# Optimization experiments

Hardware: AMD Instinct MI355X
Metric: run time of the kernel (lower is better)

Reference implementation:

```python
import jax, jax.numpy as jnp
import numpy as np

B, C, H, W = 8, 128, 64, 64


def setup_inputs() -> dict:
    key = jax.random.key(0)
    ks = jax.random.split(key, 4)
    s = 1.0 / np.sqrt(C)
    return {
        "x": jax.random.normal(ks[0], (B, C, H, W), dtype=jnp.float32),
        "Wq": jax.random.normal(ks[1], (C, C), dtype=jnp.float32) * s,
        "bq": jnp.zeros((C,), dtype=jnp.float32),
        "Wk": jax.random.normal(ks[2], (C, C), dtype=jnp.float32) * s,
        "bk": jnp.zeros((C,), dtype=jnp.float32),
        "Wv": jax.random.normal(ks[3], (C, C), dtype=jnp.float32) * s,
        "bv": jnp.zeros((C,), dtype=jnp.float32),
    }


def reference(x, Wq, bq, Wk, bk, Wv, bv):
    b, c, h, w = x.shape
    xf = x.reshape(b, c, h * w)  # [B, C, N]
    # 1x1 convs are per-pixel CxC matmuls (weight[out,in] contracted over in)
    q = jnp.einsum("oc,bcn->bon", Wq, xf) + bq[None, :, None]
    k = jnp.einsum("oc,bcn->bon", Wk, xf) + bk[None, :, None]
    v = jnp.einsum("oc,bcn->bon", Wv, xf) + bv[None, :, None]
    scale = 1.0 / jnp.sqrt(jnp.asarray(c, dtype=x.dtype))
    attn = jnp.einsum("bcn,bcm->bnm", q, k) * scale  # [B, N, N]
    attn = jax.nn.softmax(attn, axis=-1)
    out = jnp.einsum("bnm,bcm->bcn", attn, v)  # [B, C, N]
    return out.reshape(b, c, h, w) + x
```

## Files before the change

### kernel.cpp

```cpp
#include <hip/hip_runtime.h>

#define B_ 8
#define C_ 128
#define N_ 4096
#define SCALE 0.08838834764831845f

typedef __attribute__((ext_vector_type(8))) short short8;
typedef __attribute__((ext_vector_type(4))) short short4v;
typedef __attribute__((ext_vector_type(4))) float f32x4;

__device__ inline unsigned short f2b(float f) {
    unsigned int u;
    asm("v_cvt_pk_bf16_f32 %0, %1, %2" : "=v"(u) : "v"(f), "v"(f));
    return (unsigned short)u;
}

__device__ inline void gld_lds16(const void* g, void* l) {
    __builtin_amdgcn_global_load_lds(
        (const __attribute__((address_space(1))) unsigned int*)g,
        (__attribute__((address_space(3))) unsigned int*)l, 16, 0, 0);
}

__global__ __launch_bounds__(512) void kv_mfma(
    const float* __restrict__ x,
    const float* __restrict__ Wk, const float* __restrict__ bk,
    const float* __restrict__ Wv, const float* __restrict__ bv,
    unsigned short* __restrict__ kTs, unsigned short* __restrict__ vS)
{
    __shared__ __align__(16) short Xs[64 * 128];
    __shared__ __align__(16) float Obuf[64 * 132];

    const int t    = threadIdx.x;
    const int w    = t >> 6;
    const int lane = t & 63;
    const int l15  = lane & 15;
    const int quad = lane >> 4;

    const int b  = blockIdx.x & 7;
    const int n0 = (blockIdx.x >> 3) * 64;
    const long base = (long)b * C_ * N_;

    auto load_af = [&](const float* __restrict__ W, short8 (&af)[4]) {
        const int o = 16 * w + l15;
        #pragma unroll
        for (int ks = 0; ks < 4; ++ks) {
            const float4 a0 = *(const float4*)(const void*)(W + o * C_ + ks * 32 + quad * 8);
            const float4 a1 = *(const float4*)(const void*)(W + o * C_ + ks * 32 + quad * 8 + 4);
            union { unsigned int u[4]; short8 s; } pk;
            asm("v_cvt_pk_bf16_f32 %0, %1, %2" : "=v"(pk.u[0]) : "v"(a0.x), "v"(a0.y));
            asm("v_cvt_pk_bf16_f32 %0, %1, %2" : "=v"(pk.u[1]) : "v"(a0.z), "v"(a0.w));
            asm("v_cvt_pk_bf16_f32 %0, %1, %2" : "=v"(pk.u[2]) : "v"(a1.x), "v"(a1.y));
            asm("v_cvt_pk_bf16_f32 %0, %1, %2" : "=v"(pk.u[3]) : "v"(a1.z), "v"(a1.w));
            af[ks] = pk.s;
        }
    };

    auto mfma_pass = [&](const short8 (&af)[4], f32x4 (&acc)[4]) {
        #pragma unroll
        for (int nt = 0; nt < 4; ++nt) acc[nt] = (f32x4){0.f, 0.f, 0.f, 0.f};
        #pragma unroll
        for (int nt = 0; nt < 4; ++nt) {
            const int n = nt * 16 + l15;
            #pragma unroll
            for (int ks = 0; ks < 4; ++ks) {
                const short8 bx = *(const short8*)(const void*)(Xs + n * 128 + (((ks * 4 + quad) ^ l15) << 3));
                acc[nt] = __builtin_amdgcn_mfma_f32_16x16x32_bf16(af[ks], bx, acc[nt], 0, 0, 0);
            }
        }
    };

    short8 afA[4], afB[4];
    load_af(Wv, afA);

    #pragma unroll
    for (int it = 0; it < 4; ++it) {
        const int c  = (t >> 4) + it * 32;
        const int n4 = (t & 15) * 4;
        const float4 xv = *(const float4*)(const void*)(x + base + (long)c * N_ + n0 + n4);
        const int bc = c >> 3, cl = c & 7;
        Xs[(n4 + 0) * 128 + ((bc ^ ((n4 + 0) & 15)) << 3) + cl] = (short)f2b(xv.x);
        Xs[(n4 + 1) * 128 + ((bc ^ ((n4 + 1) & 15)) << 3) + cl] = (short)f2b(xv.y);
        Xs[(n4 + 2) * 128 + ((bc ^ ((n4 + 2) & 15)) << 3) + cl] = (short)f2b(xv.z);
        Xs[(n4 + 3) * 128 + ((bc ^ ((n4 + 3) & 15)) << 3) + cl] = (short)f2b(xv.w);
    }
    __syncthreads();

    {
        load_af(Wk, afB);
        f32x4 acc[4];
        mfma_pass(afA, acc);
        #pragma unroll
        for (int r = 0; r < 4; ++r) {
            const int o = 16 * w + quad * 4 + r;
            const float bb = bv[o];
            const int sw = ((o >> 1) & 3) << 3;
            #pragma unroll
            for (int nt = 0; nt < 4; ++nt) {
                const int n = nt * 16 + l15;
                const int ns = (n & 32) | ((((n >> 3) & 3) << 3) ^ sw) | (n & 7);
                vS[base + (long)o * N_ + n0 + ns] = f2b(acc[nt][r] + bb);
            }
        }
    }

    {
        f32x4 acc[4];
        mfma_pass(afB, acc);
        #pragma unroll
        for (int r = 0; r < 4; ++r) {
            const int o = 16 * w + quad * 4 + r;
            const float bb = bk[o];
            #pragma unroll
            for (int nt = 0; nt < 4; ++nt) {
                const int n = nt * 16 + l15;
                Obuf[n * 132 + (((o >> 3) ^ l15) << 3) + (o & 7)] = acc[nt][r] + bb;
            }
        }
        __syncthreads();
        const int n = t >> 3, oh = (t & 7) * 16;
        #pragma unroll
        for (int i = 0; i < 16; i += 8) {
            const float4 k0 = *(const float4*)(const void*)(Obuf + n * 132 + oh + i);
            const float4 k1 = *(const float4*)(const void*)(Obuf + n * 132 + oh + i + 4);
            union { unsigned int u[4]; short8 s; } pk;
            asm("v_cvt_pk_bf16_f32 %0, %1, %2" : "=v"(pk.u[0]) : "v"(k0.x), "v"(k0.y));
            asm("v_cvt_pk_bf16_f32 %0, %1, %2" : "=v"(pk.u[1]) : "v"(k0.z), "v"(k0.w));
            asm("v_cvt_pk_bf16_f32 %0, %1, %2" : "=v"(pk.u[2]) : "v"(k1.x), "v"(k1.y));
            asm("v_cvt_pk_bf16_f32 %0, %1, %2" : "=v"(pk.u[3]) : "v"(k1.z), "v"(k1.w));
            *(short8*)(void*)(kTs + base + (long)(n0 + n) * C_ + oh + i) = pk.s;
        }
    }
}

__global__ __launch_bounds__(512, 4) void attn_mfma(
    const float* __restrict__ Wq, const float* __restrict__ bq,
    const unsigned short* __restrict__ kTs,
    const unsigned short* __restrict__ vS,
    const float* __restrict__ xg,
    float* out)
{
    __shared__ union {
        struct {
            short V[2][2][4096];
            short Pb[2][2][2][32 * 40];
        } s;
        struct {
            short Xst[64 * 128];
            short Qs[64 * 128];
        } pre;
        float Ot[64 * 130];
    } sm;
    __shared__ float Ls[2][2][32];
    __shared__ float linvA[64];

    const int t    = threadIdx.x;
    const int w    = t >> 6;
    const int g    = w >> 2;
    const int wq   = (w >> 1) & 1;
    const int h    = w & 1;
    const int sub  = w & 3;
    const int lane = t & 63;
    const int l15  = lane & 15;
    const int quad = lane >> 4;

    const int b  = blockIdx.x & 7;
    const int n0 = (blockIdx.x >> 3) * 64;
    const long base = (long)b * C_ * N_;

    #pragma unroll
    for (int it = 0; it < 4; ++it) {
        const int c  = (t >> 4) + it * 32;
        const int n4 = (t & 15) * 4;
        const float4 xv = *(const float4*)(const void*)(xg + base + (long)c * N_ + n0 + n4);
        const int bc = c >> 3, cl = c & 7;
        sm.pre.Xst[(n4 + 0) * 128 + ((bc ^ ((n4 + 0) & 15)) << 3) + cl] = (short)f2b(xv.x);
        sm.pre.Xst[(n4 + 1) * 128 + ((bc ^ ((n4 + 1) & 15)) << 3) + cl] = (short)f2b(xv.y);
        sm.pre.Xst[(n4 + 2) * 128 + ((bc ^ ((n4 + 2) & 15)) << 3) + cl] = (short)f2b(xv.z);
        sm.pre.Xst[(n4 + 3) * 128 + ((bc ^ ((n4 + 3) & 15)) << 3) + cl] = (short)f2b(xv.w);
    }
    __syncthreads();
    {
        short8 aq[4];
        const int o = 16 * w + l15;
        #pragma unroll
        for (int ks = 0; ks < 4; ++ks) {
            const float4 a0 = *(const float4*)(const void*)(Wq + o * C_ + ks * 32 + quad * 8);
            const float4 a1 = *(const float4*)(const void*)(Wq + o * C_ + ks * 32 + quad * 8 + 4);
            union { unsigned int u[4]; short8 s; } pk;
            asm("v_cvt_pk_bf16_f32 %0, %1, %2" : "=v"(pk.u[0]) : "v"(a0.x), "v"(a0.y));
            asm("v_cvt_pk_bf16_f32 %0, %1, %2" : "=v"(pk.u[1]) : "v"(a0.z), "v"(a0.w));
            asm("v_cvt_pk_bf16_f32 %0, %1, %2" : "=v"(pk.u[2]) : "v"(a1.x), "v"(a1.y));
            asm("v_cvt_pk_bf16_f32 %0, %1, %2" : "=v"(pk.u[3]) : "v"(a1.z), "v"(a1.w));
            aq[ks] = pk.s;
        }
        f32x4 qa[4];
        #pragma unroll
        for (int nt = 0; nt < 4; ++nt) qa[nt] = (f32x4){0.f, 0.f, 0.f, 0.f};
        #pragma unroll
        for (int nt = 0; nt < 4; ++nt) {
            const int n = nt * 16 + l15;
            #pragma unroll
            for (int ks = 0; ks < 4; ++ks) {
                const short8 bx = *(const short8*)(const void*)(
                    sm.pre.Xst + n * 128 + (((ks * 4 + quad) ^ l15) << 3));
                qa[nt] = __builtin_amdgcn_mfma_f32_16x16x32_bf16(aq[ks], bx, qa[nt], 0, 0, 0);
            }
        }
        const float4 bb = *(const float4*)(const void*)(bq + 16 * w + quad * 4);
        #pragma unroll
        for (int r = 0; r < 4; ++r) {
            const int oo = 16 * w + quad * 4 + r;
            const float br = r == 0 ? bb.x : r == 1 ? bb.y : r == 2 ? bb.z : bb.w;
            #pragma unroll
            for (int nt = 0; nt < 4; ++nt) {
                const int n = nt * 16 + l15;
                sm.pre.Qs[n * 128 + (((oo >> 3) ^ (n & 15)) << 3) + (oo & 7)] =
                    (short)f2b((qa[nt][r] + br) * SCALE);
            }
        }
    }
    __syncthreads();

    short8 qf[2][4];
    #pragma unroll
    for (int qh = 0; qh < 2; ++qh)
        #pragma unroll
        for (int ks = 0; ks < 4; ++ks) {
            const int query = 32 * wq + qh * 16 + l15;
            qf[qh][ks] = *(const short8*)(const void*)(
                sm.pre.Qs + query * 128 + (((ks * 4 + quad) ^ l15) << 3));
        }

    f32x4 acc[2][4];
    #pragma unroll
    for (int qh = 0; qh < 2; ++qh)
        #pragma unroll
        for (int ct = 0; ct < 4; ++ct) acc[qh][ct] = (f32x4){0.f, 0.f, 0.f, 0.f};
    f32x4 accS[2];
    accS[0] = (f32x4){0.f, 0.f, 0.f, 0.f};
    accS[1] = (f32x4){0.f, 0.f, 0.f, 0.f};
    short8 ones;
    #pragma unroll
    for (int j = 0; j < 8; ++j) ones[j] = (short)0x3F80;

    auto stageV = [&](int buf, int pair) {
        const int mt = pair * 2 + g;
        char* lV = (char*)sm.s.V[buf][g];
        #pragma unroll
        for (int jj = 0; jj < 2; ++jj) {
            const int d  = sub * 2048 + jj * 1024;
            const int dv = d + lane * 16;
            const int c  = dv >> 6;
            gld_lds16((const char*)(vS + base + (long)c * N_ + mt * 32) + (dv & 63), lV + d);
        }
    };

    const unsigned short* kp = kTs + base + (long)((g * 32 + h * 16 + l15) * C_);
    int ko[4];
    #pragma unroll
    for (int ks = 0; ks < 4; ++ks) ko[ks] = (((ks * 4 + quad) ^ l15) << 3);
    short8 kf[4];

    stageV(0, 0);
    #pragma unroll
    for (int ks = 0; ks < 4; ++ks) kf[ks] = *(const short8*)(const void*)(kp + ko[ks]);
    kp += 64 * C_;

    for (int i = 0; i < 64; ++i) {
        f32x4 sc[2];
        sc[0] = (f32x4){0.f, 0.f, 0.f, 0.f};
        sc[1] = (f32x4){0.f, 0.f, 0.f, 0.f};
        __builtin_amdgcn_s_setprio(1);
        #pragma unroll
        for (int qh = 0; qh < 2; ++qh)
            #pragma unroll
            for (int ks = 0; ks < 4; ++ks)
                sc[qh] = __builtin_amdgcn_mfma_f32_16x16x32_bf16(qf[qh][ks], kf[ks], sc[qh], 0, 0, 0);
        __builtin_amdgcn_s_setprio(0);

        if (i < 63) {
            #pragma unroll
            for (int ks = 0; ks < 4; ++ks) kf[ks] = *(const short8*)(const void*)(kp + ko[ks]);
            kp += 64 * C_;
        }

        short* Pw = sm.s.Pb[i & 1][g][wq];
        #pragma unroll
        for (int qh = 0; qh < 2; ++qh)
            #pragma unroll
            for (int r = 0; r < 4; ++r)
                Pw[(qh * 16 + quad * 4 + r) * 40 + h * 16 + l15] = (short)f2b(__expf(sc[qh][r]));

        if (i < 63) asm volatile("s_waitcnt vmcnt(4)" ::: "memory");
        else        asm volatile("s_waitcnt vmcnt(0)" ::: "memory");
        asm volatile("s_waitcnt lgkmcnt(0)" ::: "memory");
        __builtin_amdgcn_s_barrier();
        __builtin_amdgcn_sched_barrier(0);

        if (i < 63) stageV((i + 1) & 1, i + 1);

        const short* Vb = sm.s.V[i & 1][g];
        const short8 pf0 = *(const short8*)(const void*)(Pw + (l15) * 40 + quad * 8);
        const short8 pf1 = *(const short8*)(const void*)(Pw + (16 + l15) * 40 + quad * 8);
        __builtin_amdgcn_s_setprio(1);
        if (h == 0) {
            accS[0] = __builtin_amdgcn_mfma_f32_16x16x32_bf16(pf0, ones, accS[0], 0, 0, 0);
            accS[1] = __builtin_amdgcn_mfma_f32_16x16x32_bf16(pf1, ones, accS[1], 0, 0, 0);
        }
        #pragma unroll
        for (int ct = 0; ct < 4; ++ct) {
            const int ch = h * 64 + ct * 16 + l15;
            const short8 vf = *(const short8*)(const void*)(Vb + ch * 32 + ((quad ^ ((l15 >> 1) & 3)) << 3));
            acc[0][ct] = __builtin_amdgcn_mfma_f32_16x16x32_bf16(pf0, vf, acc[0][ct], 0, 0, 0);
            acc[1][ct] = __builtin_amdgcn_mfma_f32_16x16x32_bf16(pf1, vf, acc[1][ct], 0, 0, 0);
        }
        __builtin_amdgcn_s_setprio(0);
    }

    if (h == 0 && l15 == 0) {
        #pragma unroll
        for (int qh = 0; qh < 2; ++qh)
            #pragma unroll
            for (int r = 0; r < 4; ++r)
                Ls[g][wq][qh * 16 + quad * 4 + r] = accS[qh][r];
    }
    __syncthreads();
    if (g == 0) {
        #pragma unroll
        for (int qh = 0; qh < 2; ++qh)
            #pragma unroll
            for (int ct = 0; ct < 4; ++ct)
                #pragma unroll
                for (int r = 0; r < 4; ++r)
                    sm.Ot[(32 * wq + qh * 16 + quad * 4 + r) * 130 + h * 64 + ct * 16 + l15] = acc[qh][ct][r];
    }
    __syncthreads();
    if (g == 1) {
        #pragma unroll
        for (int qh = 0; qh < 2; ++qh)
            #pragma unroll
            for (int ct = 0; ct < 4; ++ct)
                #pragma unroll
                for (int r = 0; r < 4; ++r)
                    sm.Ot[(32 * wq + qh * 16 + quad * 4 + r) * 130 + h * 64 + ct * 16 + l15] += acc[qh][ct][r];
    } else if (h == 0 && l15 == 0) {
        #pragma unroll
        for (int qh = 0; qh < 2; ++qh)
            #pragma unroll
            for (int r = 0; r < 4; ++r) {
                const int r32 = qh * 16 + quad * 4 + r;
                linvA[32 * wq + r32] = 1.0f / fmaxf(Ls[0][wq][r32] + Ls[1][wq][r32], 1e-20f);
            }
    }
    __syncthreads();

    const int c  = t >> 2;
    const int nh = (t & 3) * 16;
    const long gb = base + (long)c * N_ + n0 + nh;
    #pragma unroll
    for (int i = 0; i < 16; i += 4) {
        const float4 xs = *(const float4*)(const void*)(xg + gb + i);
        float4 rv;
        rv.x = sm.Ot[(nh + i + 0) * 130 + c] * linvA[nh + i + 0] + xs.x;
        rv.y = sm.Ot[(nh + i + 1) * 130 + c] * linvA[nh + i + 1] + xs.y;
        rv.z = sm.Ot[(nh + i + 2) * 130 + c] * linvA[nh + i + 2] + xs.z;
        rv.w = sm.Ot[(nh + i + 3) * 130 + c] * linvA[nh + i + 3] + xs.w;
        *(float4*)(void*)(out + gb + i) = rv;
    }
}

extern "C" void kernel_launch(void* const* d_in, const int* in_sizes, int n_in,
                              void* d_out, int out_size, void* d_ws, size_t ws_size,
                              hipStream_t stream) {
    const float* x  = (const float*)d_in[0];
    const float* Wq = (const float*)d_in[1];
    const float* bq = (const float*)d_in[2];
    const float* Wk = (const float*)d_in[3];
    const float* bk = (const float*)d_in[4];
    const float* Wv = (const float*)d_in[5];
    const float* bv = (const float*)d_in[6];
    float* out = (float*)d_out;

    const long BCN = (long)B_ * C_ * N_;
    unsigned short* kTs = (unsigned short*)d_ws;
    unsigned short* vS  = kTs + BCN;

    kv_mfma<<<512, 512, 0, stream>>>(x, Wk, bk, Wv, bv, kTs, vS);
    attn_mfma<<<B_ * (N_ / 64), 512, 0, stream>>>(Wq, bq, kTs, vS, x, out);
}
```

Measured before the change: 185.5 us.

## Fuse K/V projection and attention into one kernel with grid barrier

Merges the K/V projection kernel and the attention kernel into a single persistent launch of 512 blocks. Each block converts its x tile to bf16 once and reuses it for the K, V and Q projections, then all blocks meet at an atomic-counter grid barrier before attention begins. This saves a kernel launch and the second load and conversion of x, but adds a memset launch, a global spin barrier, and a dependency on all 512 blocks being resident at once to avoid deadlock.

```diff
diff --git a/kernel.cpp b/kernel.cpp
--- a/kernel.cpp
+++ b/kernel.cpp
@@ -4,6 +4,7 @@
 #define C_ 128
 #define N_ 4096
 #define SCALE 0.08838834764831845f
+#define NBLK 512u
 
 typedef __attribute__((ext_vector_type(8))) short short8;
 typedef __attribute__((ext_vector_type(4))) short short4v;
@@ -21,17 +22,38 @@
         (__attribute__((address_space(3))) unsigned int*)l, 16, 0, 0);
 }
 
-__global__ __launch_bounds__(512) void kv_mfma(
+__global__ __launch_bounds__(512, 4) void fused_attn(
     const float* __restrict__ x,
+    const float* __restrict__ Wq, const float* __restrict__ bq,
     const float* __restrict__ Wk, const float* __restrict__ bk,
     const float* __restrict__ Wv, const float* __restrict__ bv,
-    unsigned short* __restrict__ kTs, unsigned short* __restrict__ vS)
+    unsigned short* __restrict__ kTs, unsigned short* __restrict__ vS,
+    unsigned int* gsync,
+    float* __restrict__ out)
 {
-    __shared__ __align__(16) short Xs[64 * 128];
-    __shared__ __align__(16) float Obuf[64 * 132];
+    __shared__ __align__(16) union {
+        struct {
+            short Xs[64 * 128];
+            union {
+                float Obuf[64 * 132];
+                short Qs[64 * 128];
+            } o;
+        } p;
+        struct {
+            short V[2][2][4096];
+            short Pb[2][2][2][32 * 40];
+        } s;
+        float Ot[64 * 130];
+    } sm;
+    __shared__ float Ls[2][2][32];
+    __shared__ float linvA[64];
 
     const int t    = threadIdx.x;
     const int w    = t >> 6;
+    const int g    = w >> 2;
+    const int wq   = (w >> 1) & 1;
+    const int h    = w & 1;
+    const int sub  = w & 3;
     const int lane = t & 63;
     const int l15  = lane & 15;
     const int quad = lane >> 4;
@@ -63,7 +85,8 @@
             const int n = nt * 16 + l15;
             #pragma unroll
             for (int ks = 0; ks < 4; ++ks) {
-                const short8 bx = *(const short8*)(const void*)(Xs + n * 128 + (((ks * 4 + quad) ^ l15) << 3));
+                const short8 bx = *(const short8*)(const void*)(
+                    sm.p.Xs + n * 128 + (((ks * 4 + quad) ^ l15) << 3));
                 acc[nt] = __builtin_amdgcn_mfma_f32_16x16x32_bf16(af[ks], bx, acc[nt], 0, 0, 0);
             }
         }
@@ -78,10 +101,10 @@
         const int n4 = (t & 15) * 4;
         const float4 xv = *(const float4*)(const void*)(x + base + (long)c * N_ + n0 + n4);
         const int bc = c >> 3, cl = c & 7;
-        Xs[(n4 + 0) * 128 + ((bc ^ ((n4 + 0) & 15)) << 3) + cl] = (short)f2b(xv.x);
-        Xs[(n4 + 1) * 128 + ((bc ^ ((n4 + 1) & 15)) << 3) + cl] = (short)f2b(xv.y);
-        Xs[(n4 + 2) * 128 + ((bc ^ ((n4 + 2) & 15)) << 3) + cl] = (short)f2b(xv.z);
-        Xs[(n4 + 3) * 128 + ((bc ^ ((n4 + 3) & 15)) << 3) + cl] = (short)f2b(xv.w);
+        sm.p.Xs[(n4 + 0) * 128 + ((bc ^ ((n4 + 0) & 15)) << 3) + cl] = (short)f2b(xv.x);
+        sm.p.Xs[(n4 + 1) * 128 + ((bc ^ ((n4 + 1) & 15)) << 3) + cl] = (short)f2b(xv.y);
+        sm.p.Xs[(n4 + 2) * 128 + ((bc ^ ((n4 + 2) & 15)) << 3) + cl] = (short)f2b(xv.z);
+        sm.p.Xs[(n4 + 3) * 128 + ((bc ^ ((n4 + 3) & 15)) << 3) + cl] = (short)f2b(xv.w);
     }
     __syncthreads();
 
@@ -113,15 +136,15 @@
             #pragma unroll
             for (int nt = 0; nt < 4; ++nt) {
                 const int n = nt * 16 + l15;
-                Obuf[n * 132 + (((o >> 3) ^ l15) << 3) + (o & 7)] = acc[nt][r] + bb;
+                sm.p.o.Obuf[n * 132 + (((o >> 3) ^ l15) << 3) + (o & 7)] = acc[nt][r] + bb;
             }
         }
         __syncthreads();
         const int n = t >> 3, oh = (t & 7) * 16;
         #pragma unroll
         for (int i = 0; i < 16; i += 8) {
-            const float4 k0 = *(const float4*)(const void*)(Obuf + n * 132 + oh + i);
-            const float4 k1 = *(const float4*)(const void*)(Obuf + n * 132 + oh + i + 4);
+            const float4 k0 = *(const float4*)(const void*)(sm.p.o.Obuf + n * 132 + oh + i);
+            const float4 k1 = *(const float4*)(const void*)(sm.p.o.Obuf + n * 132 + oh + i + 4);
             union { unsigned int u[4]; short8 s; } pk;
             asm("v_cvt_pk_bf16_f32 %0, %1, %2" : "=v"(pk.u[0]) : "v"(k0.x), "v"(k0.y));
             asm("v_cvt_pk_bf16_f32 %0, %1, %2" : "=v"(pk.u[1]) : "v"(k0.z), "v"(k0.w));
@@ -130,69 +153,11 @@
             *(short8*)(void*)(kTs + base + (long)(n0 + n) * C_ + oh + i) = pk.s;
         }
     }
-}
-
-__global__ __launch_bounds__(512, 4) void attn_mfma(
-    const float* __restrict__ Wq, const float* __restrict__ bq,
-    const unsigned short* __restrict__ kTs,
-    const unsigned short* __restrict__ vS,
-    const float* __restrict__ xg,
-    float* out)
-{
-    __shared__ union {
-        struct {
-            short V[2][2][4096];
-            short Pb[2][2][2][32 * 40];
-        } s;
-        struct {
-            short Xst[64 * 128];
-            short Qs[64 * 128];
-        } pre;
-        float Ot[64 * 130];
-    } sm;
-    __shared__ float Ls[2][2][32];
-    __shared__ float linvA[64];
-
-    const int t    = threadIdx.x;
-    const int w    = t >> 6;
-    const int g    = w >> 2;
-    const int wq   = (w >> 1) & 1;
-    const int h    = w & 1;
-    const int sub  = w & 3;
-    const int lane = t & 63;
-    const int l15  = lane & 15;
-    const int quad = lane >> 4;
-
-    const int b  = blockIdx.x & 7;
-    const int n0 = (blockIdx.x >> 3) * 64;
-    const long base = (long)b * C_ * N_;
-
-    #pragma unroll
-    for (int it = 0; it < 4; ++it) {
-        const int c  = (t >> 4) + it * 32;
-        const int n4 = (t & 15) * 4;
-        const float4 xv = *(const float4*)(const void*)(xg + base + (long)c * N_ + n0 + n4);
-        const int bc = c >> 3, cl = c & 7;
-        sm.pre.Xst[(n4 + 0) * 128 + ((bc ^ ((n4 + 0) & 15)) << 3) + cl] = (short)f2b(xv.x);
-        sm.pre.Xst[(n4 + 1) * 128 + ((bc ^ ((n4 + 1) & 15)) << 3) + cl] = (short)f2b(xv.y);
-        sm.pre.Xst[(n4 + 2) * 128 + ((bc ^ ((n4 + 2) & 15)) << 3) + cl] = (short)f2b(xv.z);
-        sm.pre.Xst[(n4 + 3) * 128 + ((bc ^ ((n4 + 3) & 15)) << 3) + cl] = (short)f2b(xv.w);
-    }
-    __syncthreads();
+    __syncthreads();
+
     {
         short8 aq[4];
-        const int o = 16 * w + l15;
-        #pragma unroll
-        for (int ks = 0; ks < 4; ++ks) {
-            const float4 a0 = *(const float4*)(const void*)(Wq + o * C_ + ks * 32 + quad * 8);
-            const float4 a1 = *(const float4*)(const void*)(Wq + o * C_ + ks * 32 + quad * 8 + 4);
-            union { unsigned int u[4]; short8 s; } pk;
-            asm("v_cvt_pk_bf16_f32 %0, %1, %2" : "=v"(pk.u[0]) : "v"(a0.x), "v"(a0.y));
-            asm("v_cvt_pk_bf16_f32 %0, %1, %2" : "=v"(pk.u[1]) : "v"(a0.z), "v"(a0.w));
-            asm("v_cvt_pk_bf16_f32 %0, %1, %2" : "=v"(pk.u[2]) : "v"(a1.x), "v"(a1.y));
-            asm("v_cvt_pk_bf16_f32 %0, %1, %2" : "=v"(pk.u[3]) : "v"(a1.z), "v"(a1.w));
-            aq[ks] = pk.s;
-        }
+        load_af(Wq, aq);
         f32x4 qa[4];
         #pragma unroll
         for (int nt = 0; nt < 4; ++nt) qa[nt] = (f32x4){0.f, 0.f, 0.f, 0.f};
@@ -202,7 +167,7 @@
             #pragma unroll
             for (int ks = 0; ks < 4; ++ks) {
                 const short8 bx = *(const short8*)(const void*)(
-                    sm.pre.Xst + n * 128 + (((ks * 4 + quad) ^ l15) << 3));
+                    sm.p.Xs + n * 128 + (((ks * 4 + quad) ^ l15) << 3));
                 qa[nt] = __builtin_amdgcn_mfma_f32_16x16x32_bf16(aq[ks], bx, qa[nt], 0, 0, 0);
             }
         }
@@ -214,7 +179,7 @@
             #pragma unroll
             for (int nt = 0; nt < 4; ++nt) {
                 const int n = nt * 16 + l15;
-                sm.pre.Qs[n * 128 + (((oo >> 3) ^ (n & 15)) << 3) + (oo & 7)] =
+                sm.p.o.Qs[n * 128 + (((oo >> 3) ^ (n & 15)) << 3) + (oo & 7)] =
                     (short)f2b((qa[nt][r] + br) * SCALE);
             }
         }
@@ -228,8 +193,19 @@
         for (int ks = 0; ks < 4; ++ks) {
             const int query = 32 * wq + qh * 16 + l15;
             qf[qh][ks] = *(const short8*)(const void*)(
-                sm.pre.Qs + query * 128 + (((ks * 4 + quad) ^ l15) << 3));
-        }
+                sm.p.o.Qs + query * 128 + (((ks * 4 + quad) ^ l15) << 3));
+        }
+
+    __syncthreads();
+    if (t == 0) {
+        __threadfence();
+        atomicAdd(gsync, 1u);
+        while (__hip_atomic_load(gsync, __ATOMIC_ACQUIRE,
+                                 __HIP_MEMORY_SCOPE_AGENT) < NBLK)
+            __builtin_amdgcn_s_sleep(1);
+    }
+    __syncthreads();
+    __threadfence();
 
     f32x4 acc[2][4];
     #pragma unroll
@@ -359,7 +335,7 @@
     const long gb = base + (long)c * N_ + n0 + nh;
     #pragma unroll
     for (int i = 0; i < 16; i += 4) {
-        const float4 xs = *(const float4*)(const void*)(xg + gb + i);
+        const float4 xs = *(const float4*)(const void*)(x + gb + i);
         float4 rv;
         rv.x = sm.Ot[(nh + i + 0) * 130 + c] * linvA[nh + i + 0] + xs.x;
         rv.y = sm.Ot[(nh + i + 1) * 130 + c] * linvA[nh + i + 1] + xs.y;
@@ -384,7 +360,9 @@
     const long BCN = (long)B_ * C_ * N_;
     unsigned short* kTs = (unsigned short*)d_ws;
     unsigned short* vS  = kTs + BCN;
-
-    kv_mfma<<<512, 512, 0, stream>>>(x, Wk, bk, Wv, bv, kTs, vS);
-    attn_mfma<<<B_ * (N_ / 64), 512, 0, stream>>>(Wq, bq, kTs, vS, x, out);
+    unsigned int* gsync = (unsigned int*)(vS + BCN);
+
+    hipMemsetAsync((void*)gsync, 0, sizeof(unsigned int), stream);
+    fused_attn<<<dim3(NBLK), dim3(512), 0, stream>>>(
+        x, Wq, bq, Wk, bk, Wv, bv, kTs, vS, gsync, out);
 }
```

New measurement: 298.3 us. 1.61x slower.
